# Performance work log

Hardware: AMD Instinct MI355X
Metric: run time of the kernel (lower is better)

## Reference

```python
import jax, jax.numpy as jnp
import numpy as np

LN_EPS = 1e-5

def _gru_layer(x, W_ih, W_hh, b_ih, b_hh):
    # x: [B,S,Din]; W_ih: [3H,Din]; W_hh: [3H,H]; biases: [3H]
    B = x.shape[0]
    H = W_hh.shape[1]
    # Precompute input-side gate projections for all timesteps (one big GEMM).
    gx = jnp.einsum('bsd,gd->bsg', x, W_ih) + b_ih  # [B,S,3H]
    Whh_T = W_hh.T  # [H,3H]

    def step(h, gx_t):
        gh = h @ Whh_T + b_hh                     # [B,3H]
        xr, xz, xn = jnp.split(gx_t, 3, axis=-1)
        hr, hz, hn = jnp.split(gh, 3, axis=-1)
        r = jax.nn.sigmoid(xr + hr)
        z = jax.nn.sigmoid(xz + hz)
        n = jnp.tanh(xn + r * hn)
        h_new = (1.0 - z) * n + z * h
        return h_new, h_new

    h0 = jnp.zeros((B, H), dtype=x.dtype)
    h_last, ys = jax.lax.scan(step, h0, jnp.swapaxes(gx, 0, 1))  # ys: [S,B,H]
    return jnp.swapaxes(ys, 0, 1), h_last


def setup_inputs() -> dict:
    key = jax.random.key(0)
    ks = jax.random.split(key, 12)
    B, S, D, H = 256, 512, 64, 256
    L = 3
    s_in = 1.0 / np.sqrt(H)
    return {
        'x': jax.random.normal(ks[0], (B, S, D), dtype=jnp.float32),
        'W_ih0': jax.random.uniform(ks[1], (3 * H, D), jnp.float32, -s_in, s_in),
        'W_ih_rest': jax.random.uniform(ks[2], (L - 1, 3 * H, H), jnp.float32, -s_in, s_in),
        'W_hh': jax.random.uniform(ks[3], (L, 3 * H, H), jnp.float32, -s_in, s_in),
        'b_ih': jax.random.uniform(ks[4], (L, 3 * H), jnp.float32, -s_in, s_in),
        'b_hh': jax.random.uniform(ks[5], (L, 3 * H), jnp.float32, -s_in, s_in),
        'ln_gamma': jnp.ones((H,), jnp.float32),
        'ln_beta': jnp.zeros((H,), jnp.float32),
        'W1': jax.random.uniform(ks[6], (32, H), jnp.float32, -s_in, s_in),
        'b1': jax.random.uniform(ks[7], (32,), jnp.float32, -s_in, s_in),
        'W2': jax.random.uniform(ks[8], (1, 32), jnp.float32, -1 / np.sqrt(32), 1 / np.sqrt(32)),
        'b2': jax.random.uniform(ks[9], (1,), jnp.float32, -1 / np.sqrt(32), 1 / np.sqrt(32)),
    }


def reference(x, W_ih0, W_ih_rest, W_hh, b_ih, b_hh, ln_gamma, ln_beta, W1, b1, W2, b2):
    # Multi-layer GRU (batch_first), eval mode (dropout inactive).
    h = x
    L = W_hh.shape[0]
    h_last = None
    for l in range(L):
        W_ih_l = W_ih0 if l == 0 else W_ih_rest[l - 1]
        h, h_last = _gru_layer(h, W_ih_l, W_hh[l], b_ih[l], b_hh[l])
    last = h_last  # == out[:, -1, :]  [B,H]
    # LayerNorm
    mu = jnp.mean(last, axis=-1, keepdims=True)
    var = jnp.mean(jnp.square(last - mu), axis=-1, keepdims=True)
    last = (last - mu) * jax.lax.rsqrt(var + LN_EPS) * ln_gamma + ln_beta
    # MLP head
    hdn = jax.nn.relu(last @ W1.T + b1)
    pred = hdn @ W2.T + b2  # [B,1]
    return pred[:, 0]
```

## Files before the change

kernel.cpp:

```cpp
#include <hip/hip_runtime.h>
#include <stdint.h>

#define B_  256
#define S_  512
#define D_  64
#define H_  256
#define G3_ 768

typedef __attribute__((ext_vector_type(8))) short s8v;
typedef __attribute__((ext_vector_type(4))) short s4v;
typedef __attribute__((ext_vector_type(4))) float f4v;
typedef __attribute__((ext_vector_type(4))) float f4r;

#define MF(a, b, c) __builtin_amdgcn_mfma_f32_16x16x32_bf16((a), (b), (c), 0, 0, 0)

__device__ __forceinline__ unsigned short f2bf(float x) {
  unsigned u = __float_as_uint(x);
  unsigned r = (u + 0x7fffu + ((u >> 16) & 1u)) >> 16;
  return (unsigned short)r;
}
__device__ __forceinline__ float sigm(float x) {
  return __builtin_amdgcn_rcpf(1.f + __expf(-x));
}
__device__ __forceinline__ float tanh_f(float x) {
  return 1.f - 2.f * __builtin_amdgcn_rcpf(1.f + __expf(2.f * x));
}

__global__ __launch_bounds__(64) void pack_whh(
    const float* __restrict__ Whh, unsigned short* __restrict__ Whp,
    const float* __restrict__ bih, const float* __restrict__ bhh,
    float* __restrict__ bias2)
{
  const int gti = blockIdx.x, kc = blockIdx.y, lane = threadIdx.x;
  const int rowp = gti * 16 + (lane & 15);
  const int k0  = kc * 32 + (lane >> 4) * 8;
  const float* src = &Whh[(size_t)rowp * H_ + k0];
  unsigned short hi8[8];
  #pragma unroll
  for (int s = 0; s < 8; ++s) hi8[s] = f2bf(src[s]);
  const size_t o = ((size_t)(gti * 8 + kc) * 64 + lane) * 8;
  *(s8v*)&Whp[o] = *(s8v*)hi8;

  if (gti == 0 && kc == 0) {
    #pragma unroll
    for (int i = 0; i < 12; ++i) {
      int g = i * 64 + lane;
      bias2[g] = bih[g] + (g < 512 ? bhh[g] : 0.f);
    }
  }
}

__global__ __launch_bounds__(1024, 4) void fused_step(
    int s, int CH, int chsh, int cpl,
    const float* __restrict__ x, float* __restrict__ y,
    const float* __restrict__ W_ih0, const float* __restrict__ W_ihr,
    const unsigned short* __restrict__ Whp, const float* __restrict__ bhh_all,
    const float* __restrict__ bias2, float* __restrict__ gxbase,
    float* __restrict__ hbuf)
{
  const int tid = threadIdx.x;
  const int wid = tid >> 6, lane = tid & 63;
  const int fr = lane & 15, fq = lane >> 4;
  const size_t gx_elems = (size_t)B_ * CH * G3_;

  extern __shared__ unsigned short lds_[];

  if (blockIdx.x < 48) {
    const int l = blockIdx.x >> 4;
    const int c = s - 2 * l;
    if (c < 0 || c >= cpl) return;

    const unsigned short* Whp_s = Whp + (size_t)l * G3_ * H_;
    const float* bhh_s = bhh_all + (size_t)l * G3_;
    float* hb = hbuf + (size_t)l * B_ * H_;
    const float* gx_r = gxbase + (size_t)(2 * l + (c & 1)) * gx_elems;
    const int t0s = c * CH;
    const int lastL = (l == 2) ? 1 : 0;

    unsigned short* WhN  = lds_;
    unsigned short* Abuf = lds_ + 65536;

    const int bid = blockIdx.x & 15;
    const int b0  = bid * 16;
    const int bb  = fr;

    const s8v* WhpV = (const s8v*)Whp_s;

    s8v whr[8], whz[8];
    #pragma unroll
    for (int kc = 0; kc < 8; ++kc) {
      whr[kc] = WhpV[((     wid) * 8 + kc) * 64 + lane];
      whz[kc] = WhpV[((16 + wid) * 8 + kc) * 64 + lane];
    }
    #pragma unroll
    for (int kc = 0; kc < 8; ++kc) {
      s8v v = WhpV[((32 + wid) * 8 + kc) * 64 + lane];
      *(s8v*)&WhN[(wid * 8 + kc) * 512 + lane * 8] = v;
    }

    const int u0 = 16 * wid + 4 * fq;
    const f4r bhn4 = *(const f4r*)&bhh_s[2 * H_ + u0];

    f4r hn4 = {0.f, 0.f, 0.f, 0.f};
    if (t0s != 0) hn4 = *(const f4r*)&hb[(size_t)(b0 + bb) * H_ + u0];

    const int kcw  = wid >> 1;
    const int lp   = bb | (((2 * wid + (fq >> 1)) & 3) << 4);
    const int eo   = (fq & 1) * 4;
    const int aoff = kcw * 512 + lp * 8 + eo;

    {
      s4v hh;
      #pragma unroll
      for (int j = 0; j < 4; ++j) hh[j] = (short)f2bf(hn4[j]);
      *(s4v*)&Abuf[aoff] = hh;
    }

    const float* gb0 = gx_r + ((size_t)(b0 + bb) * CH) * G3_;
    f4r xr4 = *(const f4r*)(gb0 + u0);
    f4r xz4 = *(const f4r*)(gb0 + H_ + u0);
    f4r xn4 = *(const f4r*)(gb0 + 2 * H_ + u0);

    int cur = 0;
    for (int t = 0; t < CH; ++t) {
      __syncthreads();

      const int tn = (t + 1 < CH) ? t + 1 : t;
      const float* gbn = gx_r + ((size_t)(b0 + bb) * CH + tn) * G3_;
      f4r xr_n = *(const f4r*)(gbn + u0);
      f4r xz_n = *(const f4r*)(gbn + H_ + u0);
      f4r xn_n = *(const f4r*)(gbn + 2 * H_ + u0);

      f4v accR = {}, accZ = {}, accN = {};
      #pragma unroll
      for (int kc = 0; kc < 8; ++kc) {
        s8v ahh = *(const s8v*)&Abuf[cur * 4096 + kc * 512 + lane * 8];
        s8v wn  = *(const s8v*)&WhN[(wid * 8 + kc) * 512 + lane * 8];
        accR = MF(whr[kc], ahh, accR);
        accZ = MF(whz[kc], ahh, accZ);
        accN = MF(wn,      ahh, accN);
      }

      #pragma unroll
      for (int i = 0; i < 4; ++i) {
        const float r = sigm(xr4[i] + accR[i]);
        const float z = sigm(xz4[i] + accZ[i]);
        const float n = tanh_f(xn4[i] + r * (accN[i] + bhn4[i]));
        hn4[i] = (1.f - z) * n + z * hn4[i];
      }
      if (!lastL) {
        __builtin_nontemporal_store(
            hn4, (f4r*)&y[((size_t)(b0 + bb) * S_ + (t0s + t)) * H_ + u0]);
      }
      {
        s4v hh;
        #pragma unroll
        for (int j = 0; j < 4; ++j) hh[j] = (short)f2bf(hn4[j]);
        *(s4v*)&Abuf[(cur ^ 1) * 4096 + aoff] = hh;
      }
      xr4 = xr_n; xz4 = xz_n; xn4 = xn_n;
      cur ^= 1;
    }

    *(f4r*)&hb[(size_t)(b0 + bb) * H_ + u0] = hn4;

  } else {
    const int g = blockIdx.x - 48;
    const int per = CH * 12;
    const int l = g / per;
    if (l >= 3) return;
    const int c2 = s + 1 - 2 * l;
    if (c2 < 0 || c2 >= cpl) return;

    const int gidx  = g % per;
    const int mtile = gidx / 12, gtile = gidx % 12;
    const int r0 = mtile * 256, g0 = gtile * 64;

    const float* A    = (l == 0) ? x : y;
    const int    K    = (l == 0) ? D_ : H_;
    const float* Wih  = (l == 0) ? W_ih0 : (W_ihr + (size_t)(l - 1) * G3_ * H_);
    const float* b2g  = bias2 + l * 768;
    float* gx_w = gxbase + (size_t)(2 * l + (c2 & 1)) * gx_elems;
    const int t0g = c2 * CH;

    unsigned short* Ah = lds_;
    unsigned short* Wh = lds_ + 10240;

    const int row = tid >> 2;
    const int ks  = (tid & 3) * 8;
    const int CHm1 = CH - 1;
    const int r = r0 + row;
    const int rg = ((r >> chsh) * S_) + t0g + (r & CHm1);
    const float* ap = A + (size_t)rg * K + ks;
    const float* wp = Wih + (size_t)(g0 + (row & 63)) * K + ks;

    f4v acc[4] = {};

    for (int k0 = 0; k0 < K; k0 += 32) {
      float4 a0 = *(const float4*)(ap + k0);
      float4 a1 = *(const float4*)(ap + k0 + 4);
      float4 w0, w1;
      if (tid < 256) {
        w0 = *(const float4*)(wp + k0);
        w1 = *(const float4*)(wp + k0 + 4);
      }
      __syncthreads();
      {
        float av[8] = {a0.x,a0.y,a0.z,a0.w,a1.x,a1.y,a1.z,a1.w};
        unsigned short ah8[8];
        #pragma unroll
        for (int i = 0; i < 8; ++i) ah8[i] = f2bf(av[i]);
        *(s8v*)&Ah[row * 40 + ks] = *(s8v*)ah8;
        if (tid < 256) {
          float wv[8] = {w0.x,w0.y,w0.z,w0.w,w1.x,w1.y,w1.z,w1.w};
          unsigned short wh8[8];
          #pragma unroll
          for (int i = 0; i < 8; ++i) wh8[i] = f2bf(wv[i]);
          *(s8v*)&Wh[row * 40 + ks] = *(s8v*)wh8;
        }
      }
      __syncthreads();

      s8v a_hi = *(const s8v*)&Ah[(16 * wid + fr) * 40 + fq * 8];
      #pragma unroll
      for (int c = 0; c < 4; ++c) {
        s8v b_hi = *(const s8v*)&Wh[(c * 16 + fr) * 40 + fq * 8];
        acc[c] = MF(a_hi, b_hi, acc[c]);
      }
    }

    const int orow = r0 + wid * 16 + fq * 4;
    #pragma unroll
    for (int c = 0; c < 4; ++c) {
      const float bi = b2g[g0 + c * 16 + fr];
      #pragma unroll
      for (int i = 0; i < 4; ++i) {
        gx_w[(size_t)(orow + i) * G3_ + g0 + c * 16 + fr] = acc[c][i] + bi;
      }
    }
  }
}

__global__ __launch_bounds__(64) void head_kernel(
    const float* __restrict__ hlast, const float* __restrict__ lng,
    const float* __restrict__ lnb, const float* __restrict__ W1,
    const float* __restrict__ b1, const float* __restrict__ W2,
    const float* __restrict__ b2, float* __restrict__ out)
{
  const int b = blockIdx.x;
  const int lane = threadIdx.x;
  float4 v = *(const float4*)&hlast[(size_t)b * H_ + lane * 4];
  float s = v.x + v.y + v.z + v.w;
  #pragma unroll
  for (int m = 32; m > 0; m >>= 1) s += __shfl_xor(s, m, 64);
  const float mu = s * (1.f / 256.f);
  const float dx = v.x - mu, dy = v.y - mu, dz = v.z - mu, dw = v.w - mu;
  float q = dx*dx + dy*dy + dz*dz + dw*dw;
  #pragma unroll
  for (int m = 32; m > 0; m >>= 1) q += __shfl_xor(q, m, 64);
  const float rstd = rsqrtf(q * (1.f / 256.f) + 1e-5f);

  __shared__ float ln[256];
  const int i4 = lane * 4;
  ln[i4 + 0] = dx * rstd * lng[i4 + 0] + lnb[i4 + 0];
  ln[i4 + 1] = dy * rstd * lng[i4 + 1] + lnb[i4 + 1];
  ln[i4 + 2] = dz * rstd * lng[i4 + 2] + lnb[i4 + 2];
  ln[i4 + 3] = dw * rstd * lng[i4 + 3] + lnb[i4 + 3];
  __syncthreads();

  float hd = 0.f;
  if (lane < 32) {
    const float* w = W1 + (size_t)lane * H_;
    float a = 0.f;
    for (int k = 0; k < H_; ++k) a += ln[k] * w[k];
    a += b1[lane];
    hd = fmaxf(a, 0.f) * W2[lane];
  }
  #pragma unroll
  for (int m = 16; m > 0; m >>= 1) hd += __shfl_xor(hd, m, 64);
  if (lane == 0) out[b] = hd + b2[0];
}

extern "C" void kernel_launch(void* const* d_in, const int* in_sizes, int n_in,
                              void* d_out, int out_size, void* d_ws, size_t ws_size,
                              hipStream_t stream)
{
  const float* x     = (const float*)d_in[0];
  const float* W_ih0 = (const float*)d_in[1];
  const float* W_ihr = (const float*)d_in[2];
  const float* W_hh  = (const float*)d_in[3];
  const float* b_ih  = (const float*)d_in[4];
  const float* b_hh  = (const float*)d_in[5];
  const float* lng   = (const float*)d_in[6];
  const float* lnb   = (const float*)d_in[7];
  const float* W1    = (const float*)d_in[8];
  const float* b1    = (const float*)d_in[9];
  const float* W2    = (const float*)d_in[10];
  const float* b2    = (const float*)d_in[11];
  float* out = (float*)d_out;

  const size_t y_elems   = (size_t)B_ * S_ * H_;
  const size_t h_elems   = (size_t)B_ * H_;
  const size_t whp_elems = (size_t)G3_ * H_;

  int CH = 64;
  while (CH > 8) {
    size_t need = (y_elems + 6 * (size_t)B_ * CH * G3_ + 3 * h_elems + 3 * 768) * 4
                + 3 * whp_elems * 2 + 4096;
    if (need <= ws_size) break;
    CH >>= 1;
  }
  const int chsh = __builtin_ctz((unsigned)CH);
  const size_t gx_elems = (size_t)B_ * CH * G3_;
  const int cpl = S_ / CH;

  float* y      = (float*)d_ws;
  float* gxbase = y + y_elems;
  float* hbuf   = gxbase + 6 * gx_elems;
  unsigned short* Whp = (unsigned short*)(hbuf + 3 * h_elems);
  float* bias2 = (float*)(Whp + 3 * whp_elems);

  const size_t lds_bytes = 131072 + 16384;
  const int grid = 48 + 3 * CH * 12;

  for (int l = 0; l < 3; ++l) {
    pack_whh<<<dim3(48, 8), 64, 0, stream>>>(
        W_hh + (size_t)l * G3_ * H_, Whp + (size_t)l * whp_elems,
        b_ih + (size_t)l * G3_, b_hh + (size_t)l * G3_, bias2 + l * 768);
  }

  for (int s = -1; s <= cpl + 3; ++s) {
    fused_step<<<grid, 1024, lds_bytes, stream>>>(
        s, CH, chsh, cpl, x, y, W_ih0, W_ihr, Whp, b_hh, bias2, gxbase, hbuf);
  }

  head_kernel<<<256, 64, 0, stream>>>(hbuf + 2 * h_elems, lng, lnb,
                                      W1, b1, W2, b2, out);
}
```

Baseline: 1.580 ms.

## Store inter-layer activations in bf16, pre-pack W_ih, drop LDS staging in input GEMM

The recurrent path now writes the layer output y as bf16 instead of fp32, halving the inter-layer activation traffic. The input-projection GEMM reads bf16 y and pre-packed bf16 W_ih directly from global memory into MFMA operands, removing the LDS staging and both __syncthreads per k-step. The default chunk size CH is reduced from 64 to 32, which doubles the number of fused_step launches. Numerics are unchanged because y was already rounded to bf16 before the MFMA, but the GEMM now relies on cache hits for the repeated weight reads.

```diff
diff --git a/kernel.cpp b/kernel.cpp
--- a/kernel.cpp
+++ b/kernel.cpp
@@ -24,6 +24,18 @@
 }
 __device__ __forceinline__ float tanh_f(float x) {
   return 1.f - 2.f * __builtin_amdgcn_rcpf(1.f + __expf(2.f * x));
+}
+
+__global__ __launch_bounds__(256) void pack_bf16(
+    const float* __restrict__ src, unsigned short* __restrict__ dst, int n8)
+{
+  const int i = blockIdx.x * 256 + threadIdx.x;
+  if (i >= n8) return;
+  const float4 f0 = *(const float4*)(src + (size_t)i * 8);
+  const float4 f1 = *(const float4*)(src + (size_t)i * 8 + 4);
+  unsigned short h[8] = { f2bf(f0.x), f2bf(f0.y), f2bf(f0.z), f2bf(f0.w),
+                          f2bf(f1.x), f2bf(f1.y), f2bf(f1.z), f2bf(f1.w) };
+  *(s8v*)&dst[(size_t)i * 8] = *(s8v*)h;
 }
 
 __global__ __launch_bounds__(64) void pack_whh(
@@ -52,8 +64,8 @@
 
 __global__ __launch_bounds__(1024, 4) void fused_step(
     int s, int CH, int chsh, int cpl,
-    const float* __restrict__ x, float* __restrict__ y,
-    const float* __restrict__ W_ih0, const float* __restrict__ W_ihr,
+    const float* __restrict__ x, unsigned short* __restrict__ ybf,
+    const unsigned short* __restrict__ wihp,
     const unsigned short* __restrict__ Whp, const float* __restrict__ bhh_all,
     const float* __restrict__ bias2, float* __restrict__ gxbase,
     float* __restrict__ hbuf)
@@ -148,16 +160,14 @@
         const float n = tanh_f(xn4[i] + r * (accN[i] + bhn4[i]));
         hn4[i] = (1.f - z) * n + z * hn4[i];
       }
+      s4v hh;
+      #pragma unroll
+      for (int j = 0; j < 4; ++j) hh[j] = (short)f2bf(hn4[j]);
       if (!lastL) {
         __builtin_nontemporal_store(
-            hn4, (f4r*)&y[((size_t)(b0 + bb) * S_ + (t0s + t)) * H_ + u0]);
-      }
-      {
-        s4v hh;
-        #pragma unroll
-        for (int j = 0; j < 4; ++j) hh[j] = (short)f2bf(hn4[j]);
-        *(s4v*)&Abuf[(cur ^ 1) * 4096 + aoff] = hh;
-      }
+            hh, (s4v*)&ybf[((size_t)(b0 + bb) * S_ + (t0s + t)) * H_ + u0]);
+      }
+      *(s4v*)&Abuf[(cur ^ 1) * 4096 + aoff] = hh;
       xr4 = xr_n; xz4 = xz_n; xn4 = xn_n;
       cur ^= 1;
     }
@@ -176,56 +186,46 @@
     const int mtile = gidx / 12, gtile = gidx % 12;
     const int r0 = mtile * 256, g0 = gtile * 64;
 
-    const float* A    = (l == 0) ? x : y;
-    const int    K    = (l == 0) ? D_ : H_;
-    const float* Wih  = (l == 0) ? W_ih0 : (W_ihr + (size_t)(l - 1) * G3_ * H_);
-    const float* b2g  = bias2 + l * 768;
+    const int    K   = (l == 0) ? D_ : H_;
+    const unsigned short* Wp =
+        (l == 0) ? wihp : (wihp + 49152 + (size_t)(l - 1) * 196608);
+    const float* b2g = bias2 + l * 768;
     float* gx_w = gxbase + (size_t)(2 * l + (c2 & 1)) * gx_elems;
     const int t0g = c2 * CH;
 
-    unsigned short* Ah = lds_;
-    unsigned short* Wh = lds_ + 10240;
-
-    const int row = tid >> 2;
-    const int ks  = (tid & 3) * 8;
-    const int CHm1 = CH - 1;
+    const int row = 16 * wid + fr;
     const int r = r0 + row;
-    const int rg = ((r >> chsh) * S_) + t0g + (r & CHm1);
-    const float* ap = A + (size_t)rg * K + ks;
-    const float* wp = Wih + (size_t)(g0 + (row & 63)) * K + ks;
+    const int rg = ((r >> chsh) * S_) + t0g + (r & (CH - 1));
+
+    const unsigned short* wp0 = Wp + (size_t)(g0 + fr) * K + fq * 8;
 
     f4v acc[4] = {};
 
-    for (int k0 = 0; k0 < K; k0 += 32) {
-      float4 a0 = *(const float4*)(ap + k0);
-      float4 a1 = *(const float4*)(ap + k0 + 4);
-      float4 w0, w1;
-      if (tid < 256) {
-        w0 = *(const float4*)(wp + k0);
-        w1 = *(const float4*)(wp + k0 + 4);
-      }
-      __syncthreads();
-      {
-        float av[8] = {a0.x,a0.y,a0.z,a0.w,a1.x,a1.y,a1.z,a1.w};
-        unsigned short ah8[8];
+    if (l == 0) {
+      const float* apf = x + (size_t)rg * D_ + fq * 8;
+      #pragma unroll
+      for (int k0 = 0; k0 < D_; k0 += 32) {
+        float4 f0 = *(const float4*)(apf + k0);
+        float4 f1 = *(const float4*)(apf + k0 + 4);
+        unsigned short a8[8] = { f2bf(f0.x), f2bf(f0.y), f2bf(f0.z), f2bf(f0.w),
+                                 f2bf(f1.x), f2bf(f1.y), f2bf(f1.z), f2bf(f1.w) };
+        s8v a = *(s8v*)a8;
         #pragma unroll
-        for (int i = 0; i < 8; ++i) ah8[i] = f2bf(av[i]);
-        *(s8v*)&Ah[row * 40 + ks] = *(s8v*)ah8;
-        if (tid < 256) {
-          float wv[8] = {w0.x,w0.y,w0.z,w0.w,w1.x,w1.y,w1.z,w1.w};
-          unsigned short wh8[8];
-          #pragma unroll
-          for (int i = 0; i < 8; ++i) wh8[i] = f2bf(wv[i]);
-          *(s8v*)&Wh[row * 40 + ks] = *(s8v*)wh8;
+        for (int c = 0; c < 4; ++c) {
+          s8v b = *(const s8v*)(wp0 + (size_t)c * 16 * K + k0);
+          acc[c] = MF(a, b, acc[c]);
         }
       }
-      __syncthreads();
-
-      s8v a_hi = *(const s8v*)&Ah[(16 * wid + fr) * 40 + fq * 8];
-      #pragma unroll
-      for (int c = 0; c < 4; ++c) {
-        s8v b_hi = *(const s8v*)&Wh[(c * 16 + fr) * 40 + fq * 8];
-        acc[c] = MF(a_hi, b_hi, acc[c]);
+    } else {
+      const unsigned short* ap = ybf + (size_t)rg * H_ + fq * 8;
+      #pragma unroll
+      for (int k0 = 0; k0 < H_; k0 += 32) {
+        s8v a = *(const s8v*)(ap + k0);
+        #pragma unroll
+        for (int c = 0; c < 4; ++c) {
+          s8v b = *(const s8v*)(wp0 + (size_t)c * 16 * K + k0);
+          acc[c] = MF(a, b, acc[c]);
+        }
       }
     }
 
@@ -299,14 +299,16 @@
   const float* b2    = (const float*)d_in[11];
   float* out = (float*)d_out;
 
-  const size_t y_elems   = (size_t)B_ * S_ * H_;
-  const size_t h_elems   = (size_t)B_ * H_;
-  const size_t whp_elems = (size_t)G3_ * H_;
-
-  int CH = 64;
+  const size_t ybf_elems  = (size_t)B_ * S_ * H_;
+  const size_t wihp_elems = 49152 + 2 * 196608;
+  const size_t h_elems    = (size_t)B_ * H_;
+  const size_t whp_elems  = (size_t)G3_ * H_;
+
+  int CH = 32;
   while (CH > 8) {
-    size_t need = (y_elems + 6 * (size_t)B_ * CH * G3_ + 3 * h_elems + 3 * 768) * 4
-                + 3 * whp_elems * 2 + 4096;
+    size_t need = ybf_elems * 2 + wihp_elems * 2
+                + (6 * (size_t)B_ * CH * G3_ + 3 * h_elems + 3 * 768) * 4
+                + 3 * whp_elems * 2 + 8192;
     if (need <= ws_size) break;
     CH >>= 1;
   }
@@ -314,8 +316,9 @@
   const size_t gx_elems = (size_t)B_ * CH * G3_;
   const int cpl = S_ / CH;
 
-  float* y      = (float*)d_ws;
-  float* gxbase = y + y_elems;
+  unsigned short* ybf  = (unsigned short*)d_ws;
+  unsigned short* wihp = ybf + ybf_elems;
+  float* gxbase = (float*)(wihp + wihp_elems);
   float* hbuf   = gxbase + 6 * gx_elems;
   unsigned short* Whp = (unsigned short*)(hbuf + 3 * h_elems);
   float* bias2 = (float*)(Whp + 3 * whp_elems);
@@ -323,6 +326,9 @@
   const size_t lds_bytes = 131072 + 16384;
   const int grid = 48 + 3 * CH * 12;
 
+  pack_bf16<<<(49152 / 8 + 255) / 256, 256, 0, stream>>>(W_ih0, wihp, 49152 / 8);
+  pack_bf16<<<(393216 / 8 + 255) / 256, 256, 0, stream>>>(
+      W_ihr, wihp + 49152, 393216 / 8);
   for (int l = 0; l < 3; ++l) {
     pack_whh<<<dim3(48, 8), 64, 0, stream>>>(
         W_hh + (size_t)l * G3_ * H_, Whp + (size_t)l * whp_elems,
@@ -331,7 +337,7 @@
 
   for (int s = -1; s <= cpl + 3; ++s) {
     fused_step<<<grid, 1024, lds_bytes, stream>>>(
-        s, CH, chsh, cpl, x, y, W_ih0, W_ihr, Whp, b_hh, bias2, gxbase, hbuf);
+        s, CH, chsh, cpl, x, ybf, wihp, Whp, b_hh, bias2, gxbase, hbuf);
   }
 
   head_kernel<<<256, 64, 0, stream>>>(hbuf + 2 * h_elems, lng, lnb,
```

Measured after the change: 1.739 ms. 1.1x slower.
